# Performance work log

Measured on AMD Instinct MI355X. Metric: run time of the kernel, lower is better.

The kernel has to match this reference:

```python
import jax, jax.numpy as jnp
import numpy as np

N = 50000      # nodes
K = 15         # k_max candidate neighbors per node
D = 128        # node_dim
H = 64         # hidden_dim
K_MIN = 2.0
K_MAX = 15.0
TAU = 0.5      # edge_tau
LAM = 1.0      # selector_lambda


def setup_inputs() -> dict:
    key = jax.random.key(0)
    ks = jax.random.split(key, 16)
    x = jax.random.normal(ks[0], (N, D), dtype=jnp.float32)
    src = jax.random.randint(ks[1], (N * K,), 0, N)
    dst = jnp.repeat(jnp.arange(N), K)  # edges grouped by dst, as the module requires
    edge_index = jnp.stack([src, dst]).astype(jnp.int64)
    edge_dist = jax.random.uniform(ks[2], (N * K,), dtype=jnp.float32)

    def lin(k, fin, fout):
        return jax.random.normal(k, (fin, fout), dtype=jnp.float32) / np.sqrt(fin)

    EIN = 2 * D + 1  # edge MLP input: [x_dst, x_src, dist]
    return {
        "x": x, "edge_index": edge_index, "edge_dist": edge_dist,
        "ew1": lin(ks[3], EIN, H), "eb1": jnp.zeros((H,), jnp.float32),
        "ew2": lin(ks[4], H, H),   "eb2": jnp.zeros((H,), jnp.float32),
        "ew3": lin(ks[5], H, 1),   "eb3": jnp.zeros((1,), jnp.float32),
        "dw1": lin(ks[6], D + 1, H), "db1": jnp.zeros((H,), jnp.float32),
        "dw2": lin(ks[7], H, H),     "db2": jnp.zeros((H,), jnp.float32),
        "dw3": lin(ks[8], H, 1),     "db3": jnp.zeros((1,), jnp.float32),
    }


def reference(x, edge_index, edge_dist, ew1, eb1, ew2, eb2, ew3, eb3,
              dw1, db1, dw2, db2, dw3, db3):
    src_mat = edge_index[0].reshape(N, K)              # (N, K)
    x_src = x[src_mat]                                 # gather: (N, K, D)
    x_dst = jnp.broadcast_to(x[:, None, :], (N, K, D))
    edge_feat = jnp.concatenate([x_dst, x_src, edge_dist.reshape(N, K, 1)], axis=-1)

    # edge MLP -> logits (eval mode: no gumbel-logistic noise)
    h = jax.nn.relu(edge_feat @ ew1 + eb1)
    h = jax.nn.relu(h @ ew2 + eb2)
    edge_logits = (h @ ew3 + eb3)[..., 0]              # (N, K)
    edge_energy = jax.nn.sigmoid(edge_logits / TAU)

    # degree MLP -> continuous k per node
    degree_hint = edge_energy.sum(axis=1, keepdims=True)
    g = jax.nn.relu(jnp.concatenate([x, degree_hint], axis=1) @ dw1 + db1)
    g = jax.nn.relu(g @ dw2 + db2)
    k_raw = (g @ dw3 + db3)[:, 0]
    k_cont = K_MIN + (K_MAX - K_MIN) * jax.nn.sigmoid(k_raw)  # (N,)

    # per-node descending sort + straight-through top-k gate
    perm = jnp.argsort(-edge_energy, axis=1)
    energy_sorted = jnp.take_along_axis(edge_energy, perm, axis=1)
    ranks = jnp.arange(1, K + 1, dtype=x.dtype)[None, :]
    gate_soft = jax.nn.sigmoid((k_cont[:, None] - ranks) / LAM)
    k_int = jnp.clip(jnp.round(k_cont), K_MIN, K_MAX)
    gate_hard = (ranks <= k_int[:, None]).astype(gate_soft.dtype)
    gate = gate_soft + jax.lax.stop_gradient(gate_hard - gate_soft)

    gated_sorted = energy_sorted * gate
    inv_perm = jnp.argsort(perm, axis=1)               # undo the sort
    edge_gate = jnp.take_along_axis(gate, inv_perm, axis=1)
    edge_weight = jnp.take_along_axis(gated_sorted, inv_perm, axis=1)

    denom = jnp.maximum(edge_weight.sum(axis=1, keepdims=True), 1e-12)
    edge_weight = edge_weight / denom
    return (edge_weight.reshape(-1), edge_gate.reshape(-1),
            edge_energy.reshape(-1), k_cont)
```

## Files before the change

kernel.cpp:

```cpp
#include <hip/hip_runtime.h>
#include <cmath>

#define NN 50000
#define KK 15
#define DD 128
#define HH 64
#define NKE (NN * KK)

__global__ __launch_bounds__(256) void kP(const float* __restrict__ x,
                                          const float* __restrict__ ew1,
                                          const float* __restrict__ dw1,
                                          float* __restrict__ ws) {
    int lane = threadIdx.x & 63;
    int wv = __builtin_amdgcn_readfirstlane((int)(threadIdx.x >> 6));
    int seg = blockIdx.y;
    int rb = blockIdx.x * 32 + wv * 8;
    if (rb >= NN) return;
    const float* W = (seg == 0) ? ew1 : (seg == 1) ? (ew1 + 128 * HH) : dw1;
    const float* xw = x + (size_t)rb * DD;

    float acc[8];
#pragma unroll
    for (int r = 0; r < 8; ++r) acc[r] = 0.f;

#pragma unroll 1
    for (int i4 = 0; i4 < DD / 4; ++i4) {
        float xv[8][4];
#pragma unroll
        for (int r = 0; r < 8; ++r) {
            float4 v = *(const float4*)(xw + r * DD + i4 * 4);
            xv[r][0] = v.x; xv[r][1] = v.y; xv[r][2] = v.z; xv[r][3] = v.w;
        }
#pragma unroll
        for (int k = 0; k < 4; ++k) {
            float w = W[(i4 * 4 + k) * HH + lane];
#pragma unroll
            for (int r = 0; r < 8; ++r)
                acc[r] = fmaf(xv[r][k], w, acc[r]);
        }
    }
    float* o = ws + (size_t)seg * NN * HH + (size_t)rb * HH + lane;
#pragma unroll
    for (int r = 0; r < 8; ++r) o[r * HH] = acc[r];
}

__global__ __launch_bounds__(256, 1) void kE(const int* __restrict__ srcIdx,
                                             const float* __restrict__ dist,
                                             const float* __restrict__ ws,
                                             const float* __restrict__ ew1,
                                             const float* __restrict__ eb1,
                                             const float* __restrict__ ew2,
                                             const float* __restrict__ eb2,
                                             const float* __restrict__ ew3,
                                             const float* __restrict__ eb3,
                                             float* __restrict__ energy_out) {
    int t = blockIdx.x * 256 + threadIdx.x;
    int e0 = t * 2;
    if (e0 >= NKE) return;
    int s0 = srcIdx[e0], s1 = srcIdx[e0 + 1];
    int d0 = e0 / KK, d1 = (e0 + 1) / KK;
    float di0 = dist[e0], di1 = dist[e0 + 1];
    const float4* XA = (const float4*)ws;
    const float4* XB = (const float4*)(ws + (size_t)NN * HH);
    const float* w1l = ew1 + 2 * DD * HH;

    float acc0[HH], acc1[HH];
#pragma unroll
    for (int j = 0; j < HH; ++j) { acc0[j] = 0.f; acc1[j] = 0.f; }

#pragma unroll 1
    for (int i4 = 0; i4 < HH / 4; ++i4) {
        float4 a0 = XA[d0 * 16 + i4], b0 = XB[s0 * 16 + i4];
        float4 a1 = XA[d1 * 16 + i4], b1 = XB[s1 * 16 + i4];
        float av0[4] = {a0.x, a0.y, a0.z, a0.w};
        float bv0[4] = {b0.x, b0.y, b0.z, b0.w};
        float av1[4] = {a1.x, a1.y, a1.z, a1.w};
        float bv1[4] = {b1.x, b1.y, b1.z, b1.w};
        float h0[4], h1v[4];
#pragma unroll
        for (int k = 0; k < 4; ++k) {
            float wl = w1l[i4 * 4 + k];
            float bb = eb1[i4 * 4 + k];
            h0[k]  = fmaxf(av0[k] + bv0[k] + di0 * wl + bb, 0.f);
            h1v[k] = fmaxf(av1[k] + bv1[k] + di1 * wl + bb, 0.f);
        }
#pragma unroll
        for (int k = 0; k < 4; ++k) {
            const float* wr = ew2 + (i4 * 4 + k) * HH;
#pragma unroll
            for (int jj = 0; jj < 16; ++jj) {
                acc0[jj * 4 + 0] = fmaf(h0[k], wr[jj * 4 + 0], acc0[jj * 4 + 0]);
                acc0[jj * 4 + 1] = fmaf(h0[k], wr[jj * 4 + 1], acc0[jj * 4 + 1]);
                acc0[jj * 4 + 2] = fmaf(h0[k], wr[jj * 4 + 2], acc0[jj * 4 + 2]);
                acc0[jj * 4 + 3] = fmaf(h0[k], wr[jj * 4 + 3], acc0[jj * 4 + 3]);
                acc1[jj * 4 + 0] = fmaf(h1v[k], wr[jj * 4 + 0], acc1[jj * 4 + 0]);
                acc1[jj * 4 + 1] = fmaf(h1v[k], wr[jj * 4 + 1], acc1[jj * 4 + 1]);
                acc1[jj * 4 + 2] = fmaf(h1v[k], wr[jj * 4 + 2], acc1[jj * 4 + 2]);
                acc1[jj * 4 + 3] = fmaf(h1v[k], wr[jj * 4 + 3], acc1[jj * 4 + 3]);
            }
        }
    }
    float lg0 = eb3[0], lg1 = eb3[0];
#pragma unroll
    for (int j = 0; j < HH; ++j) {
        float b2 = eb2[j], w3 = ew3[j];
        lg0 = fmaf(fmaxf(acc0[j] + b2, 0.f), w3, lg0);
        lg1 = fmaf(fmaxf(acc1[j] + b2, 0.f), w3, lg1);
    }
    float2 en;
    en.x = 1.f / (1.f + expf(-2.f * lg0));
    en.y = 1.f / (1.f + expf(-2.f * lg1));
    *(float2*)(energy_out + e0) = en;
}

__global__ __launch_bounds__(128, 1) void kF(const float* __restrict__ ws,
                                             const float* __restrict__ dw1,
                                             const float* __restrict__ db1,
                                             const float* __restrict__ dw2,
                                             const float* __restrict__ db2,
                                             const float* __restrict__ dw3,
                                             const float* __restrict__ db3,
                                             float* __restrict__ out) {
    int n = blockIdx.x * 128 + threadIdx.x;
    if (n >= NN) return;
    const float* energy = out + 2 * (size_t)NKE;

    float ev[KK];
    float dh = 0.f;
#pragma unroll
    for (int j = 0; j < KK; ++j) {
        ev[j] = energy[(size_t)n * KK + j];
        dh += ev[j];
    }

    const float4* XC = (const float4*)(ws + 2 * (size_t)NN * HH);
    const float* w1l = dw1 + DD * HH;

    float acc[HH];
#pragma unroll
    for (int j = 0; j < HH; ++j) acc[j] = 0.f;

#pragma unroll 1
    for (int i4 = 0; i4 < HH / 4; ++i4) {
        float4 c = XC[n * 16 + i4];
        float cv[4] = {c.x, c.y, c.z, c.w};
#pragma unroll
        for (int k = 0; k < 4; ++k) {
            float g = fmaxf(cv[k] + dh * w1l[i4 * 4 + k] + db1[i4 * 4 + k], 0.f);
            const float* wr = dw2 + (i4 * 4 + k) * HH;
#pragma unroll
            for (int jj = 0; jj < 16; ++jj) {
                acc[jj * 4 + 0] = fmaf(g, wr[jj * 4 + 0], acc[jj * 4 + 0]);
                acc[jj * 4 + 1] = fmaf(g, wr[jj * 4 + 1], acc[jj * 4 + 1]);
                acc[jj * 4 + 2] = fmaf(g, wr[jj * 4 + 2], acc[jj * 4 + 2]);
                acc[jj * 4 + 3] = fmaf(g, wr[jj * 4 + 3], acc[jj * 4 + 3]);
            }
        }
    }
    float kraw = db3[0];
#pragma unroll
    for (int j = 0; j < HH; ++j)
        kraw = fmaf(fmaxf(acc[j] + db2[j], 0.f), dw3[j], kraw);

    float kcont = 2.f + 13.f / (1.f + expf(-kraw));
    out[3 * (size_t)NKE + n] = kcont;

    float se[16];
    int si[16];
#pragma unroll
    for (int j = 0; j < KK; ++j) { se[j] = ev[j]; si[j] = j; }
    se[15] = -1.f; si[15] = 15;

#pragma unroll
    for (int p = 1; p < 16; p <<= 1) {
#pragma unroll
        for (int k = p; k >= 1; k >>= 1) {
#pragma unroll
            for (int j = k & (p - 1); j + k < 16; j += 2 * k) {
#pragma unroll
                for (int i = 0; i < k; ++i) {
                    int a = i + j, b = i + j + k;
                    if (b < 16 && (a / (2 * p)) == (b / (2 * p))) {
                        bool sw = (se[b] > se[a]) ||
                                  (se[b] == se[a] && si[b] < si[a]);
                        float ea = sw ? se[b] : se[a];
                        float eb = sw ? se[a] : se[b];
                        int ia = sw ? si[b] : si[a];
                        int ib = sw ? si[a] : si[b];
                        se[a] = ea; se[b] = eb; si[a] = ia; si[b] = ib;
                    }
                }
            }
        }
    }

    float kint = rintf(kcont);
    kint = fminf(fmaxf(kint, 2.f), 15.f);

    float wsrt[KK];
    float denom = 0.f;
#pragma unroll
    for (int r = 0; r < KK; ++r) {
        float sel = ((float)(r + 1) <= kint) ? 1.f : 0.f;
        float wv = se[r] * sel;
        wsrt[r] = wv;
        denom += wv;
    }
    denom = fmaxf(denom, 1e-12f);

#pragma unroll
    for (int r = 0; r < KK; ++r) {
        float sel = ((float)(r + 1) <= kint) ? 1.f : 0.f;
        int j0 = si[r];
        out[(size_t)NKE + (size_t)n * KK + j0] = sel;
        out[(size_t)n * KK + j0] = wsrt[r] / denom;
    }
}

extern "C" void kernel_launch(void* const* d_in, const int* in_sizes, int n_in,
                              void* d_out, int out_size, void* d_ws, size_t ws_size,
                              hipStream_t stream) {
    const float* x   = (const float*)d_in[0];
    const int*   ei  = (const int*)d_in[1];
    const float* ed  = (const float*)d_in[2];
    const float* ew1 = (const float*)d_in[3];
    const float* eb1 = (const float*)d_in[4];
    const float* ew2 = (const float*)d_in[5];
    const float* eb2 = (const float*)d_in[6];
    const float* ew3 = (const float*)d_in[7];
    const float* eb3 = (const float*)d_in[8];
    const float* dw1 = (const float*)d_in[9];
    const float* db1 = (const float*)d_in[10];
    const float* dw2 = (const float*)d_in[11];
    const float* db2 = (const float*)d_in[12];
    const float* dw3 = (const float*)d_in[13];
    const float* db3 = (const float*)d_in[14];
    float* out = (float*)d_out;
    float* ws  = (float*)d_ws;

    hipLaunchKernelGGL(kP, dim3((NN + 31) / 32, 3), dim3(256), 0, stream,
                       x, ew1, dw1, ws);
    hipLaunchKernelGGL(kE, dim3((NKE / 2 + 255) / 256), dim3(256), 0, stream,
                       ei, ed, ws, ew1, eb1, ew2, eb2, ew3, eb3,
                       out + 2 * (size_t)NKE);
    hipLaunchKernelGGL(kF, dim3((NN + 127) / 128), dim3(128), 0, stream,
                       ws, dw1, db1, dw2, db2, dw3, db3, out);
}
```

Baseline: 325.2 us.

## Restructure all three kernels: wave-per-node edge MLP, LDS-staged inputs and weights

The edge MLP kernel now assigns one wavefront per destination node and loops over its 15 edges, with each lane holding one ew2 column in registers. The hidden vector is shared through LDS, and each edge logit is formed with a cross-lane shuffle reduction. This replaces the old scheme of two edges per thread with 128 accumulators each, which meant heavy register pressure and one block per CU. The projection kernel stages x rows in LDS once and computes all three weight segments from them. The degree kernel caches dw2 in LDS and splits its accumulators into chunks of 16. The risk is that serialising over 15 edges per wave, with LDS traffic and shuffles on every edge, adds latency per node.

```diff
diff --git a/kernel.cpp b/kernel.cpp
--- a/kernel.cpp
+++ b/kernel.cpp
@@ -11,40 +11,58 @@
                                           const float* __restrict__ ew1,
                                           const float* __restrict__ dw1,
                                           float* __restrict__ ws) {
-    int lane = threadIdx.x & 63;
-    int wv = __builtin_amdgcn_readfirstlane((int)(threadIdx.x >> 6));
-    int seg = blockIdx.y;
-    int rb = blockIdx.x * 32 + wv * 8;
-    if (rb >= NN) return;
-    const float* W = (seg == 0) ? ew1 : (seg == 1) ? (ew1 + 128 * HH) : dw1;
-    const float* xw = x + (size_t)rb * DD;
-
-    float acc[8];
-#pragma unroll
-    for (int r = 0; r < 8; ++r) acc[r] = 0.f;
-
-#pragma unroll 1
-    for (int i4 = 0; i4 < DD / 4; ++i4) {
-        float xv[8][4];
-#pragma unroll
-        for (int r = 0; r < 8; ++r) {
-            float4 v = *(const float4*)(xw + r * DD + i4 * 4);
-            xv[r][0] = v.x; xv[r][1] = v.y; xv[r][2] = v.z; xv[r][3] = v.w;
-        }
-#pragma unroll
-        for (int k = 0; k < 4; ++k) {
-            float w = W[(i4 * 4 + k) * HH + lane];
-#pragma unroll
-            for (int r = 0; r < 8; ++r)
-                acc[r] = fmaf(xv[r][k], w, acc[r]);
-        }
-    }
-    float* o = ws + (size_t)seg * NN * HH + (size_t)rb * HH + lane;
-#pragma unroll
-    for (int r = 0; r < 8; ++r) o[r * HH] = acc[r];
-}
-
-__global__ __launch_bounds__(256, 1) void kE(const int* __restrict__ srcIdx,
+    __shared__ float xs[32 * 128];
+    int tid = threadIdx.x;
+    int rb = blockIdx.x * 32;
+    int nrow = NN - rb; if (nrow > 32) nrow = 32;
+    {
+        const float4* xg = (const float4*)(x + (size_t)rb * DD);
+        float4* xs4 = (float4*)xs;
+        int nf4 = nrow * 32;
+#pragma unroll
+        for (int i = 0; i < 4; ++i) {
+            int fi = i * 256 + tid;
+            if (fi < nf4) xs4[fi] = xg[fi];
+        }
+    }
+    __syncthreads();
+
+    int lane = tid & 63;
+    int wv = tid >> 6;
+    int r0 = rb + wv * 8;
+    if (r0 >= NN) return;
+
+#pragma unroll 1
+    for (int seg = 0; seg < 3; ++seg) {
+        const float* W = (seg == 0) ? ew1 : (seg == 1) ? (ew1 + DD * HH) : dw1;
+        float acc[8];
+#pragma unroll
+        for (int r = 0; r < 8; ++r) acc[r] = 0.f;
+
+#pragma unroll 1
+        for (int i4 = 0; i4 < DD / 4; ++i4) {
+            float w0 = W[(i4 * 4 + 0) * HH + lane];
+            float w1 = W[(i4 * 4 + 1) * HH + lane];
+            float w2 = W[(i4 * 4 + 2) * HH + lane];
+            float w3 = W[(i4 * 4 + 3) * HH + lane];
+#pragma unroll
+            for (int r = 0; r < 8; ++r) {
+                float4 xv = *(const float4*)&xs[(wv * 8 + r) * 128 + i4 * 4];
+                acc[r] = fmaf(xv.x, w0, acc[r]);
+                acc[r] = fmaf(xv.y, w1, acc[r]);
+                acc[r] = fmaf(xv.z, w2, acc[r]);
+                acc[r] = fmaf(xv.w, w3, acc[r]);
+            }
+        }
+        float* o = ws + (size_t)seg * NN * HH + (size_t)r0 * HH + lane;
+#pragma unroll
+        for (int r = 0; r < 8; ++r)
+            if (r0 + r < NN) o[r * HH] = acc[r];
+    }
+}
+
+#define KE_WAVES (1536 * 4)
+__global__ __launch_bounds__(256, 4) void kE(const int* __restrict__ srcIdx,
                                              const float* __restrict__ dist,
                                              const float* __restrict__ ws,
                                              const float* __restrict__ ew1,
@@ -54,74 +72,85 @@
                                              const float* __restrict__ ew3,
                                              const float* __restrict__ eb3,
                                              float* __restrict__ energy_out) {
-    int t = blockIdx.x * 256 + threadIdx.x;
-    int e0 = t * 2;
-    if (e0 >= NKE) return;
-    int s0 = srcIdx[e0], s1 = srcIdx[e0 + 1];
-    int d0 = e0 / KK, d1 = (e0 + 1) / KK;
-    float di0 = dist[e0], di1 = dist[e0 + 1];
-    const float4* XA = (const float4*)ws;
-    const float4* XB = (const float4*)(ws + (size_t)NN * HH);
-    const float* w1l = ew1 + 2 * DD * HH;
-
-    float acc0[HH], acc1[HH];
-#pragma unroll
-    for (int j = 0; j < HH; ++j) { acc0[j] = 0.f; acc1[j] = 0.f; }
-
-#pragma unroll 1
-    for (int i4 = 0; i4 < HH / 4; ++i4) {
-        float4 a0 = XA[d0 * 16 + i4], b0 = XB[s0 * 16 + i4];
-        float4 a1 = XA[d1 * 16 + i4], b1 = XB[s1 * 16 + i4];
-        float av0[4] = {a0.x, a0.y, a0.z, a0.w};
-        float bv0[4] = {b0.x, b0.y, b0.z, b0.w};
-        float av1[4] = {a1.x, a1.y, a1.z, a1.w};
-        float bv1[4] = {b1.x, b1.y, b1.z, b1.w};
-        float h0[4], h1v[4];
-#pragma unroll
-        for (int k = 0; k < 4; ++k) {
-            float wl = w1l[i4 * 4 + k];
-            float bb = eb1[i4 * 4 + k];
-            h0[k]  = fmaxf(av0[k] + bv0[k] + di0 * wl + bb, 0.f);
-            h1v[k] = fmaxf(av1[k] + bv1[k] + di1 * wl + bb, 0.f);
-        }
-#pragma unroll
-        for (int k = 0; k < 4; ++k) {
-            const float* wr = ew2 + (i4 * 4 + k) * HH;
-#pragma unroll
-            for (int jj = 0; jj < 16; ++jj) {
-                acc0[jj * 4 + 0] = fmaf(h0[k], wr[jj * 4 + 0], acc0[jj * 4 + 0]);
-                acc0[jj * 4 + 1] = fmaf(h0[k], wr[jj * 4 + 1], acc0[jj * 4 + 1]);
-                acc0[jj * 4 + 2] = fmaf(h0[k], wr[jj * 4 + 2], acc0[jj * 4 + 2]);
-                acc0[jj * 4 + 3] = fmaf(h0[k], wr[jj * 4 + 3], acc0[jj * 4 + 3]);
-                acc1[jj * 4 + 0] = fmaf(h1v[k], wr[jj * 4 + 0], acc1[jj * 4 + 0]);
-                acc1[jj * 4 + 1] = fmaf(h1v[k], wr[jj * 4 + 1], acc1[jj * 4 + 1]);
-                acc1[jj * 4 + 2] = fmaf(h1v[k], wr[jj * 4 + 2], acc1[jj * 4 + 2]);
-                acc1[jj * 4 + 3] = fmaf(h1v[k], wr[jj * 4 + 3], acc1[jj * 4 + 3]);
-            }
-        }
-    }
-    float lg0 = eb3[0], lg1 = eb3[0];
-#pragma unroll
-    for (int j = 0; j < HH; ++j) {
-        float b2 = eb2[j], w3 = ew3[j];
-        lg0 = fmaf(fmaxf(acc0[j] + b2, 0.f), w3, lg0);
-        lg1 = fmaf(fmaxf(acc1[j] + b2, 0.f), w3, lg1);
-    }
-    float2 en;
-    en.x = 1.f / (1.f + expf(-2.f * lg0));
-    en.y = 1.f / (1.f + expf(-2.f * lg1));
-    *(float2*)(energy_out + e0) = en;
-}
-
-__global__ __launch_bounds__(128, 1) void kF(const float* __restrict__ ws,
-                                             const float* __restrict__ dw1,
-                                             const float* __restrict__ db1,
-                                             const float* __restrict__ dw2,
-                                             const float* __restrict__ db2,
-                                             const float* __restrict__ dw3,
-                                             const float* __restrict__ db3,
-                                             float* __restrict__ out) {
-    int n = blockIdx.x * 128 + threadIdx.x;
+    __shared__ float hbuf[4 * 64];
+    int lane = threadIdx.x & 63;
+    int wv = threadIdx.x >> 6;
+    float* hb = hbuf + wv * 64;
+    const float* XA = ws;
+    const float* XB = ws + (size_t)NN * HH;
+
+    float w2col[64];
+#pragma unroll
+    for (int k = 0; k < 64; ++k) w2col[k] = ew2[k * HH + lane];
+    float w1l_l = ew1[2 * DD * HH + lane];
+    float eb1_l = eb1[lane];
+    float eb2_l = eb2[lane];
+    float ew3_l = ew3[lane];
+    float eb3s = eb3[0];
+
+    int wgid = blockIdx.x * 4 + wv;
+#pragma unroll 1
+    for (int n = wgid; n < NN; n += KE_WAVES) {
+        float XAv = XA[(size_t)n * HH + lane];
+        int sv = 0; float dv = 0.f;
+        if (lane < KK) {
+            sv = srcIdx[n * KK + lane];
+            dv = dist[n * KK + lane];
+        }
+        float myE = 0.f;
+        int s0 = __shfl(sv, 0);
+        float xb = XB[(size_t)s0 * HH + lane];
+#pragma unroll 1
+        for (int e = 0; e < KK; ++e) {
+            float d_e = __shfl(dv, e);
+            float h = fmaxf(XAv + xb + d_e * w1l_l + eb1_l, 0.f);
+            hb[lane] = h;
+            if (e + 1 < KK) {
+                int sn = __shfl(sv, e + 1);
+                xb = XB[(size_t)sn * HH + lane];
+            }
+            float acc = 0.f;
+#pragma unroll
+            for (int k4 = 0; k4 < 16; ++k4) {
+                float4 h4 = *(const float4*)(hb + k4 * 4);
+                acc = fmaf(h4.x, w2col[k4 * 4 + 0], acc);
+                acc = fmaf(h4.y, w2col[k4 * 4 + 1], acc);
+                acc = fmaf(h4.z, w2col[k4 * 4 + 2], acc);
+                acc = fmaf(h4.w, w2col[k4 * 4 + 3], acc);
+            }
+            float v = fmaxf(acc + eb2_l, 0.f) * ew3_l;
+            v += __shfl_xor(v, 32);
+            v += __shfl_xor(v, 16);
+            v += __shfl_xor(v, 8);
+            v += __shfl_xor(v, 4);
+            v += __shfl_xor(v, 2);
+            v += __shfl_xor(v, 1);
+            float en = 1.f / (1.f + expf(-2.f * (v + eb3s)));
+            if (lane == e) myE = en;
+        }
+        if (lane < KK) energy_out[n * KK + lane] = myE;
+    }
+}
+
+__global__ __launch_bounds__(256) void kF(const float* __restrict__ ws,
+                                          const float* __restrict__ dw1,
+                                          const float* __restrict__ db1,
+                                          const float* __restrict__ dw2,
+                                          const float* __restrict__ db2,
+                                          const float* __restrict__ dw3,
+                                          const float* __restrict__ db3,
+                                          float* __restrict__ out) {
+    __shared__ float w2s[HH * HH];
+    {
+        const float4* g = (const float4*)dw2;
+        float4* s4 = (float4*)w2s;
+#pragma unroll
+        for (int i = 0; i < 4; ++i)
+            s4[i * 256 + threadIdx.x] = g[i * 256 + threadIdx.x];
+    }
+    __syncthreads();
+
+    int n = blockIdx.x * 256 + threadIdx.x;
     if (n >= NN) return;
     const float* energy = out + 2 * (size_t)NKE;
 
@@ -133,34 +162,41 @@
         dh += ev[j];
     }
 
-    const float4* XC = (const float4*)(ws + 2 * (size_t)NN * HH);
+    const float* XC = ws + 2 * (size_t)NN * HH + (size_t)n * HH;
     const float* w1l = dw1 + DD * HH;
-
-    float acc[HH];
-#pragma unroll
-    for (int j = 0; j < HH; ++j) acc[j] = 0.f;
-
-#pragma unroll 1
-    for (int i4 = 0; i4 < HH / 4; ++i4) {
-        float4 c = XC[n * 16 + i4];
-        float cv[4] = {c.x, c.y, c.z, c.w};
-#pragma unroll
-        for (int k = 0; k < 4; ++k) {
-            float g = fmaxf(cv[k] + dh * w1l[i4 * 4 + k] + db1[i4 * 4 + k], 0.f);
-            const float* wr = dw2 + (i4 * 4 + k) * HH;
-#pragma unroll
-            for (int jj = 0; jj < 16; ++jj) {
-                acc[jj * 4 + 0] = fmaf(g, wr[jj * 4 + 0], acc[jj * 4 + 0]);
-                acc[jj * 4 + 1] = fmaf(g, wr[jj * 4 + 1], acc[jj * 4 + 1]);
-                acc[jj * 4 + 2] = fmaf(g, wr[jj * 4 + 2], acc[jj * 4 + 2]);
-                acc[jj * 4 + 3] = fmaf(g, wr[jj * 4 + 3], acc[jj * 4 + 3]);
-            }
-        }
-    }
     float kraw = db3[0];
-#pragma unroll
-    for (int j = 0; j < HH; ++j)
-        kraw = fmaf(fmaxf(acc[j] + db2[j], 0.f), dw3[j], kraw);
+
+#pragma unroll 1
+    for (int c = 0; c < 4; ++c) {
+        float acc[16];
+#pragma unroll
+        for (int t = 0; t < 16; ++t) acc[t] = 0.f;
+#pragma unroll 1
+        for (int k4 = 0; k4 < 16; ++k4) {
+            float4 cx = *(const float4*)(XC + k4 * 4);
+            float cv[4] = {cx.x, cx.y, cx.z, cx.w};
+#pragma unroll
+            for (int m = 0; m < 4; ++m) {
+                int k = k4 * 4 + m;
+                float g = fmaxf(cv[m] + dh * w1l[k] + db1[k], 0.f);
+                float4 wA = *(const float4*)&w2s[k * HH + c * 16 + 0];
+                float4 wB = *(const float4*)&w2s[k * HH + c * 16 + 4];
+                float4 wC = *(const float4*)&w2s[k * HH + c * 16 + 8];
+                float4 wD = *(const float4*)&w2s[k * HH + c * 16 + 12];
+                acc[0]  = fmaf(g, wA.x, acc[0]);  acc[1]  = fmaf(g, wA.y, acc[1]);
+                acc[2]  = fmaf(g, wA.z, acc[2]);  acc[3]  = fmaf(g, wA.w, acc[3]);
+                acc[4]  = fmaf(g, wB.x, acc[4]);  acc[5]  = fmaf(g, wB.y, acc[5]);
+                acc[6]  = fmaf(g, wB.z, acc[6]);  acc[7]  = fmaf(g, wB.w, acc[7]);
+                acc[8]  = fmaf(g, wC.x, acc[8]);  acc[9]  = fmaf(g, wC.y, acc[9]);
+                acc[10] = fmaf(g, wC.z, acc[10]); acc[11] = fmaf(g, wC.w, acc[11]);
+                acc[12] = fmaf(g, wD.x, acc[12]); acc[13] = fmaf(g, wD.y, acc[13]);
+                acc[14] = fmaf(g, wD.z, acc[14]); acc[15] = fmaf(g, wD.w, acc[15]);
+            }
+        }
+#pragma unroll
+        for (int t = 0; t < 16; ++t)
+            kraw = fmaf(fmaxf(acc[t] + db2[c * 16 + t], 0.f), dw3[c * 16 + t], kraw);
+    }
 
     float kcont = 2.f + 13.f / (1.f + expf(-kraw));
     out[3 * (size_t)NKE + n] = kcont;
@@ -202,9 +238,9 @@
 #pragma unroll
     for (int r = 0; r < KK; ++r) {
         float sel = ((float)(r + 1) <= kint) ? 1.f : 0.f;
-        float wv = se[r] * sel;
-        wsrt[r] = wv;
-        denom += wv;
+        float wvv = se[r] * sel;
+        wsrt[r] = wvv;
+        denom += wvv;
     }
     denom = fmaxf(denom, 1e-12f);
 
@@ -238,11 +274,11 @@
     float* out = (float*)d_out;
     float* ws  = (float*)d_ws;
 
-    hipLaunchKernelGGL(kP, dim3((NN + 31) / 32, 3), dim3(256), 0, stream,
+    hipLaunchKernelGGL(kP, dim3((NN + 31) / 32), dim3(256), 0, stream,
                        x, ew1, dw1, ws);
-    hipLaunchKernelGGL(kE, dim3((NKE / 2 + 255) / 256), dim3(256), 0, stream,
+    hipLaunchKernelGGL(kE, dim3(1536), dim3(256), 0, stream,
                        ei, ed, ws, ew1, eb1, ew2, eb2, ew3, eb3,
                        out + 2 * (size_t)NKE);
-    hipLaunchKernelGGL(kF, dim3((NN + 127) / 128), dim3(128), 0, stream,
+    hipLaunchKernelGGL(kF, dim3((NN + 255) / 256), dim3(256), 0, stream,
                        ws, dw1, db1, dw2, db2, dw3, db3, out);
 }
```

Result: slower. 389.2 us (+19.7%).
